# Performance work log

Hardware: AMD Instinct MI355X
Metric: run time of the kernel (lower is better)

## Reference

```python
import jax, jax.numpy as jnp
import numpy as np

D_MODEL = 1024
N_HEADS = 16
HEAD_DIM = D_MODEL // N_HEADS
WINDOW = 256


def setup_inputs() -> dict:
    key = jax.random.key(0)
    ks = jax.random.split(key, 5)
    s = 1.0 / np.sqrt(D_MODEL)
    x = jax.random.normal(ks[0], (1, 4096, D_MODEL), dtype=jnp.float32)
    W_qkv = jax.random.uniform(ks[1], (D_MODEL, 3 * D_MODEL), jnp.float32, -s, s)
    b_qkv = jax.random.uniform(ks[2], (3 * D_MODEL,), jnp.float32, -s, s)
    W_proj = jax.random.uniform(ks[3], (D_MODEL, D_MODEL), jnp.float32, -s, s)
    b_proj = jax.random.uniform(ks[4], (D_MODEL,), jnp.float32, -s, s)
    return {"x": x, "W_qkv": W_qkv, "b_qkv": b_qkv, "W_proj": W_proj, "b_proj": b_proj}


def reference(x, W_qkv, b_qkv, W_proj, b_proj):
    b, t, c = x.shape
    qkv = x @ W_qkv + b_qkv  # [b,t,3c]
    q, k, v = jnp.split(qkv, 3, axis=-1)
    # [b,h,t,d]
    q = q.reshape(b, t, N_HEADS, HEAD_DIM).transpose(0, 2, 1, 3)
    k = k.reshape(b, t, N_HEADS, HEAD_DIM).transpose(0, 2, 1, 3)
    v = v.reshape(b, t, N_HEADS, HEAD_DIM).transpose(0, 2, 1, 3)
    att = jnp.einsum('bhqd,bhkd->bhqk', q, k) / np.sqrt(HEAD_DIM)
    idx = jnp.arange(t)
    diff = idx[:, None] - idx[None, :]  # query - key
    allowed = (diff >= 0) & (diff < WINDOW)  # causal & local window
    att = jnp.where(allowed[None, None], att, -jnp.inf)
    att = jax.nn.softmax(att, axis=-1)
    y = jnp.einsum('bhqk,bhkd->bhqd', att, v)
    y = y.transpose(0, 2, 1, 3).reshape(b, t, c)
    return y @ W_proj + b_proj
```

## Files before the change

kernel.cpp:

```cpp
#include <hip/hip_runtime.h>
#include <stdint.h>

#define TSEQ 4096
#define DMODEL 1024
#define N3 3072
#define NHEADS 16
#define HDIM 64
#define WINDOW 256

typedef __attribute__((ext_vector_type(8))) short short8;
typedef __attribute__((ext_vector_type(4))) float f32x4;

__device__ __forceinline__ unsigned short f2bf(float f) {
  unsigned u = __builtin_bit_cast(unsigned, f);
  return (unsigned short)((u + 0x7fffu + ((u >> 16) & 1u)) >> 16);
}

__device__ __forceinline__ unsigned cvtpk(float lo, float hi) {
  unsigned r;
  asm("v_cvt_pk_bf16_f32 %0, %1, %2" : "=v"(r) : "v"(lo), "v"(hi));
  return r;
}

__device__ __forceinline__ f32x4 mfma16(short8 a, short8 b, f32x4 c) {
  return __builtin_amdgcn_mfma_f32_16x16x32_bf16(a, b, c, 0, 0, 0);
}

__device__ __forceinline__ void g2lds16(const void* g, void* l) {
  __builtin_amdgcn_global_load_lds(
      (const __attribute__((address_space(1))) void*)(uintptr_t)g,
      (__attribute__((address_space(3))) void*)(uintptr_t)l,
      16, 0, 0);
}


__global__ __launch_bounds__(256) void prep(const float* __restrict__ x,
                                            const float* __restrict__ Wqkv,
                                            const float* __restrict__ Wproj,
                                            unsigned short* __restrict__ xb,
                                            unsigned short* __restrict__ oQkvT,
                                            unsigned short* __restrict__ oProjT) {
  __shared__ float tile[32][33];
  int b = blockIdx.x;
  int tid = threadIdx.x;
  if (b < 4096) {
    int i = (b * 256 + tid) * 4;
    float4 v = *(const float4*)(x + i);
    unsigned lo = cvtpk(v.x, v.y), hi = cvtpk(v.z, v.w);
    unsigned long long packed = (unsigned long long)lo | ((unsigned long long)hi << 32);
    *(unsigned long long*)(xb + i) = packed;
    return;
  }
  b -= 4096;
  int bx = b & 127, by = b >> 7;
  const float* in;
  unsigned short* out;
  int C;
  if (bx < 96) {
    in = Wqkv; out = oQkvT; C = N3;
  } else {
    bx -= 96; in = Wproj; out = oProjT; C = DMODEL;
  }
  const int R = DMODEL;
  int c0 = bx * 32;
  int r0 = by * 32;
  int tx = tid & 31, ty = tid >> 5;
#pragma unroll
  for (int i = 0; i < 32; i += 8)
    tile[ty + i][tx] = in[(size_t)(r0 + ty + i) * C + c0 + tx];
  __syncthreads();
#pragma unroll
  for (int i = 0; i < 32; i += 8)
    out[(size_t)(c0 + ty + i) * R + r0 + tx] = f2bf(tile[tx][ty + i]);
}


template <int EPI, int MI, int NI>
__global__ __launch_bounds__(256)
void gemm_bf16(const unsigned short* __restrict__ A,
               const unsigned short* __restrict__ BT,
               const float* __restrict__ bias,
               unsigned short* __restrict__ oQ,
               unsigned short* __restrict__ oK,
               unsigned short* __restrict__ oVT,
               float* __restrict__ oF) {
  constexpr int BM = MI * 32, BN = NI * 32;
  constexpr int LPS = MI / 2 + NI / 2;
  __shared__ unsigned short Asm[2][BM * 32];
  __shared__ unsigned short Bsm[2][BN * 32];
  const int K = 1024;
  int m0 = blockIdx.x * BM;
  int n0 = blockIdx.y * BN;
  int tid = threadIdx.x;
  int w = tid >> 6, lane = tid & 63;
  int l15 = lane & 15, l4 = lane >> 4;
  int wm = (w >> 1) * (MI * 16), wn = (w & 1) * (NI * 16);

  f32x4 acc[MI][NI];
#pragma unroll
  for (int i = 0; i < MI; i++)
#pragma unroll
    for (int j = 0; j < NI; j++) acc[i][j] = (f32x4){0.f, 0.f, 0.f, 0.f};

  int lr = lane >> 2;
  int slot = ((lane & 3) * 16) ^ (((lr >> 1) & 3) << 4);
  const char* aG = (const char*)(A + (size_t)(m0 + w * (BM / 4) + lr) * K) + slot;
  const char* bG = (const char*)(BT + (size_t)(n0 + w * (BN / 4) + lr) * K) + slot;
  const size_t rowSkip = (size_t)16 * K * 2;

  auto stage = [&](int s, int b) {
    int koff = s * 64;
#pragma unroll
    for (int j = 0; j < MI / 2; j++)
      g2lds16(aG + j * rowSkip + koff, &Asm[b][(w * (MI / 2) + j) * 512]);
#pragma unroll
    for (int j = 0; j < NI / 2; j++)
      g2lds16(bG + j * rowSkip + koff, &Bsm[b][(w * (NI / 2) + j) * 512]);
  };

  int sX = ((l15 >> 1) & 3) << 4;

  auto compute = [&](int b) {
    short8 af[MI], bfr[NI];
#pragma unroll
    for (int mi = 0; mi < MI; mi++) {
      int rA = wm + mi * 16 + l15;
      af[mi] = *(const short8*)((const char*)Asm[b] + rA * 64 + ((l4 * 16) ^ sX));
    }
#pragma unroll
    for (int ni = 0; ni < NI; ni++) {
      int rB = wn + ni * 16 + l15;
      bfr[ni] = *(const short8*)((const char*)Bsm[b] + rB * 64 + ((l4 * 16) ^ sX));
    }
#pragma unroll
    for (int mi = 0; mi < MI; mi++)
#pragma unroll
      for (int ni = 0; ni < NI; ni++)
        acc[mi][ni] = mfma16(af[mi], bfr[ni], acc[mi][ni]);
  };

  const int NS = K / 32;
  stage(0, 0);
#pragma unroll 1
  for (int s = 0; s < NS; s++) {
    if (s + 1 < NS) {
      stage(s + 1, (s + 1) & 1);
      if constexpr (LPS == 3) asm volatile("s_waitcnt vmcnt(3)" ::: "memory");
      else if constexpr (LPS == 2) asm volatile("s_waitcnt vmcnt(2)" ::: "memory");
      else asm volatile("s_waitcnt vmcnt(4)" ::: "memory");
    } else {
      asm volatile("s_waitcnt vmcnt(0)" ::: "memory");
    }
    __builtin_amdgcn_s_barrier();
    __builtin_amdgcn_sched_barrier(0);
    compute(s & 1);
    __builtin_amdgcn_sched_barrier(0);
    __builtin_amdgcn_s_barrier();
  }

#pragma unroll
  for (int ni = 0; ni < NI; ni++) {
    int nn = n0 + wn + ni * 16 + l15;
    float bv = bias[nn];
    int c = nn & 1023;
    int hh = c >> 6, dd = c & 63;
#pragma unroll
    for (int mi = 0; mi < MI; mi++) {
      int mm = m0 + wm + mi * 16 + l4 * 4;
      float v0 = acc[mi][ni][0] + bv;
      float v1 = acc[mi][ni][1] + bv;
      float v2 = acc[mi][ni][2] + bv;
      float v3 = acc[mi][ni][3] + bv;
      if (EPI == 1) {
        oF[(size_t)(mm + 0) * 1024 + nn] = v0;
        oF[(size_t)(mm + 1) * 1024 + nn] = v1;
        oF[(size_t)(mm + 2) * 1024 + nn] = v2;
        oF[(size_t)(mm + 3) * 1024 + nn] = v3;
      } else if (nn < 1024) {
        oQ[((size_t)hh * TSEQ + mm + 0) * 64 + dd] = f2bf(v0 * 0.125f);
        oQ[((size_t)hh * TSEQ + mm + 1) * 64 + dd] = f2bf(v1 * 0.125f);
        oQ[((size_t)hh * TSEQ + mm + 2) * 64 + dd] = f2bf(v2 * 0.125f);
        oQ[((size_t)hh * TSEQ + mm + 3) * 64 + dd] = f2bf(v3 * 0.125f);
      } else if (nn < 2048) {
        oK[((size_t)hh * TSEQ + mm + 0) * 64 + dd] = f2bf(v0);
        oK[((size_t)hh * TSEQ + mm + 1) * 64 + dd] = f2bf(v1);
        oK[((size_t)hh * TSEQ + mm + 2) * 64 + dd] = f2bf(v2);
        oK[((size_t)hh * TSEQ + mm + 3) * 64 + dd] = f2bf(v3);
      } else {
        unsigned lo = cvtpk(v0, v1), hi = cvtpk(v2, v3);
        unsigned long long pv = (unsigned long long)lo | ((unsigned long long)hi << 32);
        *(unsigned long long*)(oVT + ((size_t)hh * 64 + dd) * TSEQ + mm) = pv;
      }
    }
  }
}


__global__ __launch_bounds__(256)
void attn_swa(const unsigned short* __restrict__ Qa,
              const unsigned short* __restrict__ Ka,
              const unsigned short* __restrict__ Vt,
              unsigned short* __restrict__ Y) {
  __shared__ __align__(16) char KV[2][16384];
  __shared__ __align__(16) unsigned char Pl[4][2048];
  int flat = blockIdx.x;
  int swz = (flat & 7) * 128 + (flat >> 3);
  int h = swz >> 6, qb = swz & 63;
  int w = threadIdx.x >> 6, lane = threadIdx.x & 63;
  int l15 = lane & 15, l4 = lane >> 4;
  int qrow0 = qb * 64 + w * 16;
  int q = qrow0 + l15;

  const unsigned short* qp = Qa + ((size_t)h * TSEQ + q) * 64 + l4 * 8;
  short8 qf0 = *(const short8*)qp;
  short8 qf1 = *(const short8*)(qp + 32);

  const char* kgb = (const char*)(Ka + (size_t)h * TSEQ * 64);
  const char* vgb = (const char*)(Vt + (size_t)h * 64 * TSEQ);

  auto stage = [&](int kt, int b) {
    int kbase = kt * 64;
    int sub = lane >> 3, slot = (lane & 7) * 16;
    if (w < 2) {
      int R0 = w * 32;
      const char* src = kgb + (size_t)kbase * 128;
#pragma unroll
      for (int j = 0; j < 4; j++) {
        int r = R0 + j * 8 + sub;
        g2lds16(src + r * 128 + (slot ^ ((r & 7) << 4)), &KV[b][R0 * 128 + j * 1024]);
      }
    } else {
      int D0 = (w - 2) * 32;
      const char* src = vgb + (size_t)kbase * 2;
#pragma unroll
      for (int j = 0; j < 4; j++) {
        int d = D0 + j * 8 + sub;
        g2lds16(src + (size_t)d * 8192 + (slot ^ ((d & 7) << 4)),
                &KV[b][8192 + D0 * 128 + j * 1024]);
      }
    }
  };

  float m = -1e30f, lsum = 0.f;
  f32x4 o[4];
#pragma unroll
  for (int ni = 0; ni < 4; ni++) o[ni] = (f32x4){0.f, 0.f, 0.f, 0.f};

  unsigned char* pw = Pl[w];
  int xw = (l15 & 7) << 4;

  auto compute = [&](int kt, int b, int MODE) {
    int kbase = kt * 64;
    const char* kb = KV[b];
    const char* vb = KV[b] + 8192;
    f32x4 s[4];
#pragma unroll
    for (int ni = 0; ni < 4; ni++) {
      int rb = (ni * 16 + l15) * 128;
      short8 k0 = *(const short8*)(kb + rb + ((l4 * 16) ^ xw));
      short8 k1 = *(const short8*)(kb + rb + ((64 + l4 * 16) ^ xw));
      f32x4 z = (f32x4){0.f, 0.f, 0.f, 0.f};
      z = mfma16(k0, qf0, z);
      s[ni] = mfma16(k1, qf1, z);
    }
    if (MODE != 0) {
#pragma unroll
      for (int ni = 0; ni < 4; ni++)
#pragma unroll
        for (int r = 0; r < 4; r++) {
          int key = kbase + ni * 16 + l4 * 4 + r;
          bool ok = (MODE == 2) ? (key <= q) : (q - key < WINDOW);
          s[ni][r] = ok ? s[ni][r] : -1e30f;
        }
    }
    float pm0 = fmaxf(fmaxf(s[0][0], s[0][1]), fmaxf(s[0][2], s[0][3]));
    float pm1 = fmaxf(fmaxf(s[1][0], s[1][1]), fmaxf(s[1][2], s[1][3]));
    float pm2 = fmaxf(fmaxf(s[2][0], s[2][1]), fmaxf(s[2][2], s[2][3]));
    float pm3 = fmaxf(fmaxf(s[3][0], s[3][1]), fmaxf(s[3][2], s[3][3]));
    float pm = fmaxf(fmaxf(pm0, pm1), fmaxf(pm2, pm3));
    pm = fmaxf(pm, __shfl_xor(pm, 16, 64));
    pm = fmaxf(pm, __shfl_xor(pm, 32, 64));
    float mn = fmaxf(m, pm);
    float alpha = __expf(m - mn);
    m = mn;
    float rs = 0.f;
#pragma unroll
    for (int ni = 0; ni < 4; ni++)
#pragma unroll
      for (int r = 0; r < 4; r++) {
        float p = __expf(s[ni][r] - mn);
        s[ni][r] = p;
        rs += p;
      }
    rs += __shfl_xor(rs, 16, 64);
    rs += __shfl_xor(rs, 32, 64);
    lsum = lsum * alpha + rs;
#pragma unroll
    for (int ni = 0; ni < 4; ni++) {
      unsigned lo = cvtpk(s[ni][0], s[ni][1]);
      unsigned hi = cvtpk(s[ni][2], s[ni][3]);
      unsigned long long pv = (unsigned long long)lo | ((unsigned long long)hi << 32);
      *(unsigned long long*)(pw + l15 * 128 + ((ni * 32 + l4 * 8) ^ xw)) = pv;
    }
    short8 pa0 = *(const short8*)(pw + l15 * 128 + ((l4 * 16) ^ xw));
    short8 pa1 = *(const short8*)(pw + l15 * 128 + ((64 + l4 * 16) ^ xw));
#pragma unroll
    for (int ni = 0; ni < 4; ni++)
#pragma unroll
      for (int r = 0; r < 4; r++) o[ni][r] *= alpha;
#pragma unroll
    for (int ni = 0; ni < 4; ni++) {
      int rb = (ni * 16 + l15) * 128;
      short8 v0 = *(const short8*)(vb + rb + ((l4 * 16) ^ xw));
      short8 v1 = *(const short8*)(vb + rb + ((64 + l4 * 16) ^ xw));
      o[ni] = mfma16(v0, pa0, o[ni]);
      o[ni] = mfma16(v1, pa1, o[ni]);
    }
  };

  int kt0 = qb >= 4 ? qb - 4 : 0;
  int NT = qb - kt0 + 1;
  stage(kt0, 0);
  for (int t = 0; t < NT; t++) {
    int kt = kt0 + t;
    if (t + 1 < NT) {
      stage(kt + 1, (t + 1) & 1);
      asm volatile("s_waitcnt vmcnt(4)" ::: "memory");
    } else {
      asm volatile("s_waitcnt vmcnt(0)" ::: "memory");
    }
    __builtin_amdgcn_s_barrier();
    __builtin_amdgcn_sched_barrier(0);
    int MODE = (t == NT - 1) ? 2 : ((qb >= 4 && t == 0) ? 1 : 0);
    compute(kt, t & 1, MODE);
    __builtin_amdgcn_sched_barrier(0);
    __builtin_amdgcn_s_barrier();
  }

  float inv = 1.f / lsum;
#pragma unroll
  for (int ni = 0; ni < 4; ni++) {
    unsigned lo = cvtpk(o[ni][0] * inv, o[ni][1] * inv);
    unsigned hi = cvtpk(o[ni][2] * inv, o[ni][3] * inv);
    unsigned long long yv = (unsigned long long)lo | ((unsigned long long)hi << 32);
    *(unsigned long long*)(Y + (size_t)q * DMODEL + h * 64 + ni * 16 + l4 * 4) = yv;
  }
}


extern "C" void kernel_launch(void* const* d_in, const int* in_sizes, int n_in,
                              void* d_out, int out_size, void* d_ws, size_t ws_size,
                              hipStream_t stream) {
  const float* x = (const float*)d_in[0];
  const float* Wqkv = (const float*)d_in[1];
  const float* bqkv = (const float*)d_in[2];
  const float* Wproj = (const float*)d_in[3];
  const float* bproj = (const float*)d_in[4];
  float* out = (float*)d_out;

  unsigned short* ws = (unsigned short*)d_ws;
  unsigned short* xb = ws;
  unsigned short* wqkvT = xb + (size_t)TSEQ * DMODEL;
  unsigned short* wprojT = wqkvT + (size_t)N3 * DMODEL;
  unsigned short* qarr = wprojT + (size_t)DMODEL * DMODEL;
  unsigned short* karr = qarr + (size_t)NHEADS * TSEQ * HDIM;
  unsigned short* vtarr = karr + (size_t)NHEADS * TSEQ * HDIM;
  unsigned short* yarr = vtarr + (size_t)NHEADS * TSEQ * HDIM;

  prep<<<8192, 256, 0, stream>>>(x, Wqkv, Wproj, xb, wqkvT, wprojT);
  gemm_bf16<0, 4, 2><<<dim3(TSEQ / 128, N3 / 64), 256, 0, stream>>>(xb, wqkvT, bqkv, qarr, karr, vtarr, nullptr);
  attn_swa<<<1024, 256, 0, stream>>>(qarr, karr, vtarr, yarr);
  gemm_bf16<1, 2, 2><<<dim3(TSEQ / 64, DMODEL / 64), 256, 0, stream>>>(yarr, wprojT, bproj, nullptr, nullptr, nullptr, out);
}
```

Measured before the change: 93.00 us.

## Fuse x fp32-to-bf16 conversion into QKV GEMM, lazy softmax rescale, setprio

Drops the separate x-to-bf16 conversion pass. The QKV GEMM now streams fp32 x into LDS and converts it to bf16 while building fragments, which removes a full write and read of the activation. The QKV GEMM tile is widened to 4x4, and s_setprio wraps the MFMA sections in both the GEMM and the attention kernel. Attention skips the online-softmax rescale when the running max does not change. The costs are double the LDS footprint for A and extra conversion work inside the inner loop.

```diff
diff --git a/kernel.cpp b/kernel.cpp
--- a/kernel.cpp
+++ b/kernel.cpp
@@ -34,25 +34,12 @@
 }
 
 
-__global__ __launch_bounds__(256) void prep(const float* __restrict__ x,
-                                            const float* __restrict__ Wqkv,
+__global__ __launch_bounds__(256) void prep(const float* __restrict__ Wqkv,
                                             const float* __restrict__ Wproj,
-                                            unsigned short* __restrict__ xb,
                                             unsigned short* __restrict__ oQkvT,
                                             unsigned short* __restrict__ oProjT) {
   __shared__ float tile[32][33];
-  int b = blockIdx.x;
-  int tid = threadIdx.x;
-  if (b < 4096) {
-    int i = (b * 256 + tid) * 4;
-    float4 v = *(const float4*)(x + i);
-    unsigned lo = cvtpk(v.x, v.y), hi = cvtpk(v.z, v.w);
-    unsigned long long packed = (unsigned long long)lo | ((unsigned long long)hi << 32);
-    *(unsigned long long*)(xb + i) = packed;
-    return;
-  }
-  b -= 4096;
-  int bx = b & 127, by = b >> 7;
+  int bx = blockIdx.x;
   const float* in;
   unsigned short* out;
   int C;
@@ -63,7 +50,8 @@
   }
   const int R = DMODEL;
   int c0 = bx * 32;
-  int r0 = by * 32;
+  int r0 = blockIdx.y * 32;
+  int tid = threadIdx.x;
   int tx = tid & 31, ty = tid >> 5;
 #pragma unroll
   for (int i = 0; i < 32; i += 8)
@@ -75,9 +63,9 @@
 }
 
 
-template <int EPI, int MI, int NI>
+template <int EPI, bool AF32, int MI, int NI>
 __global__ __launch_bounds__(256)
-void gemm_bf16(const unsigned short* __restrict__ A,
+void gemm_bf16(const void* __restrict__ Ap,
                const unsigned short* __restrict__ BT,
                const float* __restrict__ bias,
                unsigned short* __restrict__ oQ,
@@ -85,9 +73,11 @@
                unsigned short* __restrict__ oVT,
                float* __restrict__ oF) {
   constexpr int BM = MI * 32, BN = NI * 32;
-  constexpr int LPS = MI / 2 + NI / 2;
-  __shared__ unsigned short Asm[2][BM * 32];
-  __shared__ unsigned short Bsm[2][BN * 32];
+  constexpr int ABY = AF32 ? BM * 32 * 4 : BM * 32 * 2;
+  constexpr int BBY = BN * 32 * 2;
+  constexpr int LPS = (AF32 ? MI : MI / 2) + NI / 2;
+  __shared__ __align__(16) char Asm[2][ABY];
+  __shared__ __align__(16) char Bsm[2][BBY];
   const int K = 1024;
   int m0 = blockIdx.x * BM;
   int n0 = blockIdx.y * BN;
@@ -102,41 +92,75 @@
 #pragma unroll
     for (int j = 0; j < NI; j++) acc[i][j] = (f32x4){0.f, 0.f, 0.f, 0.f};
 
-  int lr = lane >> 2;
-  int slot = ((lane & 3) * 16) ^ (((lr >> 1) & 3) << 4);
-  const char* aG = (const char*)(A + (size_t)(m0 + w * (BM / 4) + lr) * K) + slot;
-  const char* bG = (const char*)(BT + (size_t)(n0 + w * (BN / 4) + lr) * K) + slot;
-  const size_t rowSkip = (size_t)16 * K * 2;
+  const char* aG;
+  if constexpr (AF32) {
+    int sub8 = lane >> 3;
+    int slotA = ((lane & 7) ^ sub8) * 16;
+    aG = (const char*)Ap + (size_t)(m0 + w * (MI * 8) + sub8) * 4096 + slotA;
+  } else {
+    int lr = lane >> 2;
+    int slotB = ((lane & 3) * 16) ^ (((lr >> 1) & 3) << 4);
+    aG = (const char*)Ap + (size_t)(m0 + w * (MI * 8) + lr) * 2048 + slotB;
+  }
+  const char* bG;
+  {
+    int lr = lane >> 2;
+    int slotB = ((lane & 3) * 16) ^ (((lr >> 1) & 3) << 4);
+    bG = (const char*)BT + (size_t)(n0 + w * (NI * 8) + lr) * 2048 + slotB;
+  }
 
   auto stage = [&](int s, int b) {
+    if constexpr (AF32) {
+      int koff = s * 128;
+#pragma unroll
+      for (int c = 0; c < MI; c++)
+        g2lds16(aG + (size_t)c * 8 * 4096 + koff, &Asm[b][(w * MI + c) * 1024]);
+    } else {
+      int koff = s * 64;
+#pragma unroll
+      for (int c = 0; c < MI / 2; c++)
+        g2lds16(aG + (size_t)c * 16 * 2048 + koff, &Asm[b][(w * (MI / 2) + c) * 1024]);
+    }
     int koff = s * 64;
 #pragma unroll
-    for (int j = 0; j < MI / 2; j++)
-      g2lds16(aG + j * rowSkip + koff, &Asm[b][(w * (MI / 2) + j) * 512]);
-#pragma unroll
     for (int j = 0; j < NI / 2; j++)
-      g2lds16(bG + j * rowSkip + koff, &Bsm[b][(w * (NI / 2) + j) * 512]);
+      g2lds16(bG + (size_t)j * 16 * 2048 + koff, &Bsm[b][(w * (NI / 2) + j) * 1024]);
   };
 
   int sX = ((l15 >> 1) & 3) << 4;
+  int swA = (l15 & 7) << 4;
 
   auto compute = [&](int b) {
     short8 af[MI], bfr[NI];
 #pragma unroll
     for (int mi = 0; mi < MI; mi++) {
       int rA = wm + mi * 16 + l15;
-      af[mi] = *(const short8*)((const char*)Asm[b] + rA * 64 + ((l4 * 16) ^ sX));
+      if constexpr (AF32) {
+        const char* base = Asm[b] + rA * 128;
+        f32x4 lo = *(const f32x4*)(base + ((l4 * 32) ^ swA));
+        f32x4 hi = *(const f32x4*)(base + ((l4 * 32 + 16) ^ swA));
+        union { short8 s; unsigned u[4]; } t;
+        t.u[0] = cvtpk(lo[0], lo[1]);
+        t.u[1] = cvtpk(lo[2], lo[3]);
+        t.u[2] = cvtpk(hi[0], hi[1]);
+        t.u[3] = cvtpk(hi[2], hi[3]);
+        af[mi] = t.s;
+      } else {
+        af[mi] = *(const short8*)(Asm[b] + rA * 64 + ((l4 * 16) ^ sX));
+      }
     }
 #pragma unroll
     for (int ni = 0; ni < NI; ni++) {
       int rB = wn + ni * 16 + l15;
-      bfr[ni] = *(const short8*)((const char*)Bsm[b] + rB * 64 + ((l4 * 16) ^ sX));
-    }
+      bfr[ni] = *(const short8*)(Bsm[b] + rB * 64 + ((l4 * 16) ^ sX));
+    }
+    __builtin_amdgcn_s_setprio(1);
 #pragma unroll
     for (int mi = 0; mi < MI; mi++)
 #pragma unroll
       for (int ni = 0; ni < NI; ni++)
         acc[mi][ni] = mfma16(af[mi], bfr[ni], acc[mi][ni]);
+    __builtin_amdgcn_s_setprio(0);
   };
 
   const int NS = K / 32;
@@ -145,9 +169,9 @@
   for (int s = 0; s < NS; s++) {
     if (s + 1 < NS) {
       stage(s + 1, (s + 1) & 1);
-      if constexpr (LPS == 3) asm volatile("s_waitcnt vmcnt(3)" ::: "memory");
-      else if constexpr (LPS == 2) asm volatile("s_waitcnt vmcnt(2)" ::: "memory");
-      else asm volatile("s_waitcnt vmcnt(4)" ::: "memory");
+      if constexpr (LPS == 6) asm volatile("s_waitcnt vmcnt(6)" ::: "memory");
+      else if constexpr (LPS == 4) asm volatile("s_waitcnt vmcnt(4)" ::: "memory");
+      else asm volatile("s_waitcnt vmcnt(2)" ::: "memory");
     } else {
       asm volatile("s_waitcnt vmcnt(0)" ::: "memory");
     }
@@ -254,6 +278,7 @@
     const char* kb = KV[b];
     const char* vb = KV[b] + 8192;
     f32x4 s[4];
+    __builtin_amdgcn_s_setprio(1);
 #pragma unroll
     for (int ni = 0; ni < 4; ni++) {
       int rb = (ni * 16 + l15) * 128;
@@ -263,6 +288,7 @@
       z = mfma16(k0, qf0, z);
       s[ni] = mfma16(k1, qf1, z);
     }
+    __builtin_amdgcn_s_setprio(0);
     if (MODE != 0) {
 #pragma unroll
       for (int ni = 0; ni < 4; ni++)
@@ -280,21 +306,28 @@
     float pm = fmaxf(fmaxf(pm0, pm1), fmaxf(pm2, pm3));
     pm = fmaxf(pm, __shfl_xor(pm, 16, 64));
     pm = fmaxf(pm, __shfl_xor(pm, 32, 64));
-    float mn = fmaxf(m, pm);
-    float alpha = __expf(m - mn);
-    m = mn;
+    if (!__all(pm <= m)) {
+      float mn = fmaxf(m, pm);
+      float alpha = __expf(m - mn);
+      m = mn;
+      lsum *= alpha;
+#pragma unroll
+      for (int ni = 0; ni < 4; ni++)
+#pragma unroll
+        for (int r = 0; r < 4; r++) o[ni][r] *= alpha;
+    }
     float rs = 0.f;
 #pragma unroll
     for (int ni = 0; ni < 4; ni++)
 #pragma unroll
       for (int r = 0; r < 4; r++) {
-        float p = __expf(s[ni][r] - mn);
+        float p = __expf(s[ni][r] - m);
         s[ni][r] = p;
         rs += p;
       }
     rs += __shfl_xor(rs, 16, 64);
     rs += __shfl_xor(rs, 32, 64);
-    lsum = lsum * alpha + rs;
+    lsum += rs;
 #pragma unroll
     for (int ni = 0; ni < 4; ni++) {
       unsigned lo = cvtpk(s[ni][0], s[ni][1]);
@@ -304,10 +337,7 @@
     }
     short8 pa0 = *(const short8*)(pw + l15 * 128 + ((l4 * 16) ^ xw));
     short8 pa1 = *(const short8*)(pw + l15 * 128 + ((64 + l4 * 16) ^ xw));
-#pragma unroll
-    for (int ni = 0; ni < 4; ni++)
-#pragma unroll
-      for (int r = 0; r < 4; r++) o[ni][r] *= alpha;
+    __builtin_amdgcn_s_setprio(1);
 #pragma unroll
     for (int ni = 0; ni < 4; ni++) {
       int rb = (ni * 16 + l15) * 128;
@@ -316,6 +346,7 @@
       o[ni] = mfma16(v0, pa0, o[ni]);
       o[ni] = mfma16(v1, pa1, o[ni]);
     }
+    __builtin_amdgcn_s_setprio(0);
   };
 
   int kt0 = qb >= 4 ? qb - 4 : 0;
@@ -359,16 +390,17 @@
   float* out = (float*)d_out;
 
   unsigned short* ws = (unsigned short*)d_ws;
-  unsigned short* xb = ws;
-  unsigned short* wqkvT = xb + (size_t)TSEQ * DMODEL;
+  unsigned short* wqkvT = ws;
   unsigned short* wprojT = wqkvT + (size_t)N3 * DMODEL;
   unsigned short* qarr = wprojT + (size_t)DMODEL * DMODEL;
   unsigned short* karr = qarr + (size_t)NHEADS * TSEQ * HDIM;
   unsigned short* vtarr = karr + (size_t)NHEADS * TSEQ * HDIM;
   unsigned short* yarr = vtarr + (size_t)NHEADS * TSEQ * HDIM;
 
-  prep<<<8192, 256, 0, stream>>>(x, Wqkv, Wproj, xb, wqkvT, wprojT);
-  gemm_bf16<0, 4, 2><<<dim3(TSEQ / 128, N3 / 64), 256, 0, stream>>>(xb, wqkvT, bqkv, qarr, karr, vtarr, nullptr);
+  prep<<<dim3(128, 32), 256, 0, stream>>>(Wqkv, Wproj, wqkvT, wprojT);
+  gemm_bf16<0, true, 4, 4><<<dim3(TSEQ / 128, N3 / 128), 256, 0, stream>>>(
+      x, wqkvT, bqkv, qarr, karr, vtarr, nullptr);
   attn_swa<<<1024, 256, 0, stream>>>(qarr, karr, vtarr, yarr);
-  gemm_bf16<1, 2, 2><<<dim3(TSEQ / 64, DMODEL / 64), 256, 0, stream>>>(yarr, wprojT, bproj, nullptr, nullptr, nullptr, out);
-}
+  gemm_bf16<1, false, 2, 2><<<dim3(TSEQ / 64, DMODEL / 64), 256, 0, stream>>>(
+      yarr, wprojT, bproj, nullptr, nullptr, nullptr, out);
+}
```

New measurement: 87.83 us. -5.6%, faster.
